# Kernel optimization log

Measured on AMD Instinct MI355X. Metric: run time of the kernel, lower is better.

The kernel has to match this reference:

```python
import jax, jax.numpy as jnp
import numpy as np

DIM = 64
LSH_NUM_PROJS = 7
BLOCK_SIZE = 256
SAMPLE_SIZE = 256
MIN_SEQ_LEN = 2048


def _unit_hamming(n):
    # Gray-code-like permutation used by AngularLSH so adjacent hash ids differ by 1 bit
    a = np.arange(2)
    for i in range(1, n):
        a = np.concatenate([a, a[::-1] + 2 ** i])
    return jnp.asarray(a, dtype=jnp.int32)

_PERM = _unit_hamming(LSH_NUM_PROJS)                                  # [2^P]
_ENC = (2 ** jnp.arange(LSH_NUM_PROJS)).reshape(1, 1, 1, LSH_NUM_PROJS)


def _lsh_hash(mat, proj_dir):
    # mat: [b,h,n,d], proj_dir: [1,1,d,P] -> hash ids [b,h,n]
    mask = jnp.matmul(mat, proj_dir) > 0
    bin_ids = (mask * _ENC).sum(-1)
    return _PERM[bin_ids]


def _exact_attention(q, k, v, scale, causal=False, bias=None):
    qk = jnp.einsum('bhnd,bhmd->bhnm', q, k) * scale
    if causal:
        n, m = q.shape[2], k.shape[2]
        qk = qk + jnp.triu(jnp.full((n, m), jnp.finfo(q.dtype).min, q.dtype), 1)[None, None]
    if bias is not None:
        qk = qk + bias
    lse = jax.scipy.special.logsumexp(qk, axis=-1, keepdims=True)      # [b,h,n,1]
    out = jnp.einsum('bhnm,bhmd->bhnd', jnp.exp(qk - lse), v)
    return out, lse


def _add_attn(a1, l1, a2, l2):
    c = (1.0 / (1.0 + jnp.exp(l2 - l1))).astype(a1.dtype)
    attn = c * a1 + (1 - c) * a2
    lse = l1 - jnp.log(c + jnp.finfo(l1.dtype).eps)
    return attn, lse


def _indexing(x, idx, chunk_size=-1):
    # x: [b,h,n,d], idx: [b,h,s] -> [b,h,s,d] (padded up to a multiple of chunk_size)
    g = jnp.take_along_axis(x, idx[..., None], axis=2)
    n = g.shape[2]
    if chunk_size > 0 and n % chunk_size != 0:
        pad = -n % chunk_size
        g = jnp.pad(g, ((0, 0), (0, 0), (0, pad), (0, 0)))
    return g


def _no_causal(q, k, v, scale, proj_dir, level):
    b, h, n_q, d = q.shape
    n_k = k.shape[2]
    if MIN_SEQ_LEN > n_q:
        return _exact_attention(q, k, v, scale, causal=False)
    q_idx = jnp.argsort(_lsh_hash(q, proj_dir), axis=2)
    k_idx = jnp.argsort(_lsh_hash(k, proj_dir), axis=2)
    q_idx_inv = jnp.argsort(q_idx, axis=2)
    kbs = BLOCK_SIZE
    q_s = _indexing(q, q_idx, kbs)
    k_s = _indexing(k, k_idx, kbs)
    v_s = _indexing(v, k_idx, kbs)
    num_blocks = k_s.shape[2] // kbs
    qbs = q_s.shape[2] // num_blocks
    # block-diagonal attention over LSH-sorted buckets
    q_blk = q_s.reshape(-1, 1, qbs, d)
    k_blk = k_s.reshape(-1, 1, kbs, d)
    v_blk = v_s.reshape(-1, 1, kbs, d)
    attn_block, lse_block = _exact_attention(q_blk, k_blk, v_blk, scale, causal=False)
    attn_block = attn_block.reshape(b, h, q_s.shape[2], -1)
    lse_block = lse_block.reshape(b, h, q_s.shape[2], -1)
    if q_s.shape[2] != n_q:
        attn_block = attn_block[:, :, :n_q, :]
        lse_block = lse_block[:, :, :n_q, :]
        q_s = q_s[:, :, :n_q, :]
        k_s = k_s[:, :, :n_k, :]
        v_s = v_s[:, :, :n_k, :]
    S = SAMPLE_SIZE
    if S > 0 and n_q > qbs and n_k > kbs:
        rng = jax.random.fold_in(jax.random.key(42), level)
        sampled = jax.random.randint(rng, (b, h, S), 0, n_k)
        v_sub = _indexing(v_s, sampled)
        k_sub = _indexing(k_s, sampled)
        offset = jnp.arange(n_q)[None, :, None]                         # (1,n,1)
        bm = (offset // qbs) == (sampled // kbs).reshape(-1, 1, S)      # (b*h,n,S)
        bias = bm.reshape(b, h, n_q, S).astype(q_s.dtype) * jnp.finfo(q_s.dtype).min
        attn_res, lse_res = _exact_attention(q_s, k_sub, v_sub, scale, causal=False, bias=bias)
        lse_res = lse_res + jnp.asarray(np.log(n_k / S), lse_res.dtype)
        attn, lse = _add_attn(attn_block, lse_block, attn_res, lse_res)
    else:
        attn, lse = attn_block, lse_block
    attn = _indexing(attn, q_idx_inv)
    lse = _indexing(lse, q_idx_inv)
    return attn, lse


def _hyper(q, k, v, scale, proj_dir, level=0):
    b, h, n_k, d = k.shape
    n_q = q.shape[2]
    if n_k <= MIN_SEQ_LEN:
        return _exact_attention(q, k, v, scale, causal=True)
    # recursive causal split: block-diagonal halves + un-masked lower-left quadrant
    q_bd = q.reshape(b, 2 * h, n_q // 2, d)
    k_bd = k.reshape(b, 2 * h, n_k // 2, d)
    v_bd = v.reshape(b, 2 * h, n_k // 2, d)
    attn_bd, lse_bd = _hyper(q_bd, k_bd, v_bd, scale, proj_dir, level + 1)
    attn_bd = attn_bd.reshape(b, h, -1, d)
    lse_bd = lse_bd.reshape(b, h, -1, 1)
    a_un, l_un = _no_causal(q[:, :, n_k // 2:, :], k[:, :, :n_k // 2, :],
                            v[:, :, :n_k // 2, :], scale, proj_dir, 100 + level)
    a_up, l_up = attn_bd[:, :, :n_q // 2, :], lse_bd[:, :, :n_q // 2, :]
    a_dn, l_dn = _add_attn(attn_bd[:, :, n_q // 2:, :], lse_bd[:, :, n_q // 2:, :], a_un, l_un)
    return jnp.concatenate([a_up, a_dn], axis=2), jnp.concatenate([l_up, l_dn], axis=2)


def setup_inputs() -> dict:
    rng = jax.random.key(0)
    kq, kk, kv, kp = jax.random.split(rng, 4)
    B, H, N, D = 1, 8, 8192, 64
    return {
        'query': jax.random.normal(kq, (B, H, N, D), jnp.float32),
        'key': jax.random.normal(kk, (B, H, N, D), jnp.float32),
        'value': jax.random.normal(kv, (B, H, N, D), jnp.float32),
        'proj_dir': jax.random.normal(kp, (1, 1, D, LSH_NUM_PROJS), jnp.float32),
    }


def reference(query, key, value, proj_dir):
    scale = query.shape[-1] ** -0.5
    attn, lse = _hyper(query, key, value, scale, proj_dir)
    return attn
```

## Files before the change

kernel.cpp:

```cpp
#include <hip/hip_runtime.h>
#include <stdint.h>
#include <math.h>

#define H 8
#define NSEQ 8192
#define D 64
#define SC2 0.18033688011112042f
#define LN2F 0.69314718055994531f
#define THR2 10.0f
#define EPSF 1.1920928955078125e-07f

typedef short v8s __attribute__((ext_vector_type(8)));
typedef float v4f __attribute__((ext_vector_type(4)));
typedef unsigned short ushort_t;

#define MFMA16(a,b,c) __builtin_amdgcn_mfma_f32_16x16x32_bf16((a),(b),(c),0,0,0)
#define SWZ(row, cb)    (((row)*128) + ((cb) ^ ((((row)&7))<<4)))
#define SWZ256(row, cb) (((row)*256) + ((cb) ^ ((((row)&7))<<4)))

__device__ __forceinline__ float exp2x(float x){
  float r; asm("v_exp_f32 %0, %1" : "=v"(r) : "v"(x)); return r;
}
__device__ __forceinline__ unsigned int cvtpk(float a, float b){
  unsigned int r; asm("v_cvt_pk_bf16_f32 %0, %1, %2" : "=v"(r) : "v"(a), "v"(b)); return r;
}
__device__ __forceinline__ ushort_t f2bf(float f){
  union { float f; unsigned int u; } c; c.f = f;
  unsigned int u = c.u + 0x7FFFu + ((c.u >> 16) & 1u);
  return (ushort_t)(u >> 16);
}
#define VONES (v8s){0x3F80,0x3F80,0x3F80,0x3F80,0x3F80,0x3F80,0x3F80,0x3F80}

__global__ __launch_bounds__(256) void prep_hash(
    const float* __restrict__ q, const float* __restrict__ k, const float* __restrict__ v,
    const float* __restrict__ proj,
    ushort_t* __restrict__ qb, ushort_t* __restrict__ kb, ushort_t* __restrict__ vb,
    int* __restrict__ hq, int* __restrict__ hk)
{
  __shared__ float tile[64][65];
  __shared__ float pj[448];
  __shared__ int pbuf[4][64];
  const int bid = blockIdx.x;
  const int t = threadIdx.x;
  if (bid >= 2048){
    const int tix = bid - 2048;
    size_t off = (size_t)tix*4096 + t*16;
    float4 f0 = *(const float4*)(v + off);
    float4 f1 = *(const float4*)(v + off + 4);
    float4 f2 = *(const float4*)(v + off + 8);
    float4 f3 = *(const float4*)(v + off + 12);
    uint4 o0, o1;
    o0.x = cvtpk(f0.x, f0.y);  o0.y = cvtpk(f0.z, f0.w);
    o0.z = cvtpk(f1.x, f1.y);  o0.w = cvtpk(f1.z, f1.w);
    o1.x = cvtpk(f2.x, f2.y);  o1.y = cvtpk(f2.z, f2.w);
    o1.z = cvtpk(f3.x, f3.y);  o1.w = cvtpk(f3.z, f3.w);
    *(uint4*)(vb + off) = o0;
    *(uint4*)(vb + off + 8) = o1;
    return;
  }
  const int isk = bid & 1;
  const int tix = bid >> 1;
  const int rowbase = tix << 6;
  const float* src = isk ? k : q;
  ushort_t* dstb = isk ? kb : qb;
  int* dsth = isk ? hk : hq;
  for (int i = t; i < 448; i += 256) pj[i] = proj[i];
  {
    const int r = t >> 2, cg = (t & 3) << 4;
    const float* s = src + (size_t)(rowbase + r)*64 + cg;
    float4 f0 = *(const float4*)(s);
    float4 f1 = *(const float4*)(s + 4);
    float4 f2 = *(const float4*)(s + 8);
    float4 f3 = *(const float4*)(s + 12);
    tile[r][cg+0]=f0.x;  tile[r][cg+1]=f0.y;  tile[r][cg+2]=f0.z;  tile[r][cg+3]=f0.w;
    tile[r][cg+4]=f1.x;  tile[r][cg+5]=f1.y;  tile[r][cg+6]=f1.z;  tile[r][cg+7]=f1.w;
    tile[r][cg+8]=f2.x;  tile[r][cg+9]=f2.y;  tile[r][cg+10]=f2.z; tile[r][cg+11]=f2.w;
    tile[r][cg+12]=f3.x; tile[r][cg+13]=f3.y; tile[r][cg+14]=f3.z; tile[r][cg+15]=f3.w;
    uint4 o0, o1;
    o0.x = cvtpk(f0.x, f0.y);  o0.y = cvtpk(f0.z, f0.w);
    o0.z = cvtpk(f1.x, f1.y);  o0.w = cvtpk(f1.z, f1.w);
    o1.x = cvtpk(f2.x, f2.y);  o1.y = cvtpk(f2.z, f2.w);
    o1.z = cvtpk(f3.x, f3.y);  o1.w = cvtpk(f3.z, f3.w);
    *(uint4*)(dstb + (size_t)(rowbase + r)*64 + cg) = o0;
    *(uint4*)(dstb + (size_t)(rowbase + r)*64 + cg + 8) = o1;
  }
  __syncthreads();
  {
    const int r = t & 63, pg = t >> 6;
    const int p2 = (pg < 3) ? (pg + 4) : 6;
    float d0 = 0.0f, d1 = 0.0f;
    for (int d = 0; d < 64; ++d){
      float x = tile[r][d];
      d0 = fmaf(x, pj[d*7 + pg], d0);
      d1 = fmaf(x, pj[d*7 + p2], d1);
    }
    int pb = (d0 > 0.0f ? (1 << pg) : 0);
    if (pg < 3 && d1 > 0.0f) pb |= (1 << (pg + 4));
    pbuf[pg][r] = pb;
  }
  __syncthreads();
  if (t < 64){
    int b = pbuf[0][t] | pbuf[1][t] | pbuf[2][t] | pbuf[3][t];
    dsth[rowbase + t] = b ^ (b >> 1);
  }
}

__device__ __forceinline__ void tf2x32(uint32_t k0, uint32_t k1,
                                       uint32_t x0, uint32_t x1,
                                       uint32_t& o0, uint32_t& o1)
{
  uint32_t ks0 = k0, ks1 = k1, ks2 = k0 ^ k1 ^ 0x1BD11BDAu;
  x0 += ks0; x1 += ks1;
#define RND(r) { x0 += x1; x1 = (x1 << (r)) | (x1 >> (32-(r))); x1 ^= x0; }
  RND(13) RND(15) RND(26) RND(6)  x0 += ks1; x1 += ks2 + 1u;
  RND(17) RND(29) RND(16) RND(24) x0 += ks2; x1 += ks0 + 2u;
  RND(13) RND(15) RND(26) RND(6)  x0 += ks0; x1 += ks1 + 3u;
  RND(17) RND(29) RND(16) RND(24) x0 += ks1; x1 += ks2 + 4u;
  RND(13) RND(15) RND(26) RND(6)  x0 += ks2; x1 += ks0 + 5u;
#undef RND
  o0 = x0; o1 = x1;
}

__device__ __forceinline__ void qk8(const v8s qf[2], const char* Ks, int lo, int hi, v4f sa[8]){
  __builtin_amdgcn_s_setprio(1);
#pragma unroll
  for (int st = 0; st < 8; ++st){
#pragma unroll
    for (int kc = 0; kc < 2; ++kc){
      v8s bf = *(const v8s*)(Ks + SWZ(st*16 + lo, kc*64 + hi*16));
      sa[st] = MFMA16(qf[kc], bf, sa[st]);
    }
  }
  __builtin_amdgcn_s_setprio(0);
}

__device__ __forceinline__ void sm_pv8s(v4f sa[8], char* Pw, const char* VTs,
                                        int lo, int hi, float m[4], v4f o[5]){
  float tm[4];
  bool grow = false;
#pragma unroll
  for (int reg = 0; reg < 4; ++reg){
    float a = fmaxf(fmaxf(sa[0][reg], sa[1][reg]), fmaxf(sa[2][reg], sa[3][reg]));
    float b = fmaxf(fmaxf(sa[4][reg], sa[5][reg]), fmaxf(sa[6][reg], sa[7][reg]));
    tm[reg] = fmaxf(a, b);
    grow = grow || (tm[reg] > m[reg] + THR2);
  }
  if (__any(grow)){
#pragma unroll
    for (int reg = 0; reg < 4; ++reg){
      float t = tm[reg];
      t = fmaxf(t, __shfl_xor(t, 1));
      t = fmaxf(t, __shfl_xor(t, 2));
      t = fmaxf(t, __shfl_xor(t, 4));
      t = fmaxf(t, __shfl_xor(t, 8));
      float mn = fmaxf(m[reg], t);
      float corr = exp2x(m[reg] - mn);
      m[reg] = mn;
#pragma unroll
      for (int dt = 0; dt < 5; ++dt) o[dt][reg] *= corr;
    }
  }
#pragma unroll
  for (int hh = 0; hh < 2; ++hh){
#pragma unroll
    for (int reg = 0; reg < 4; ++reg){
      float mr = m[reg];
      uint2 pw;
      pw.x = cvtpk(exp2x(sa[hh*4+0][reg]-mr), exp2x(sa[hh*4+1][reg]-mr));
      pw.y = cvtpk(exp2x(sa[hh*4+2][reg]-mr), exp2x(sa[hh*4+3][reg]-mr));
      *(uint2*)(Pw + SWZ(hi*4 + reg, 8*lo)) = pw;
    }
    asm volatile("" ::: "memory");
    __builtin_amdgcn_s_setprio(1);
#pragma unroll
    for (int kb = 0; kb < 2; ++kb){
      v8s pa = *(const v8s*)(Pw + SWZ(lo, kb*64 + hi*16));
#pragma unroll
      for (int dt = 0; dt < 4; ++dt){
        v8s vbr = *(const v8s*)(VTs + SWZ256(dt*16 + lo, hh*128 + kb*64 + hi*16));
        o[dt] = MFMA16(pa, vbr, o[dt]);
      }
      o[4] = MFMA16(pa, VONES, o[4]);
    }
    __builtin_amdgcn_s_setprio(0);
    asm volatile("" ::: "memory");
  }
}

__device__ __forceinline__ void vt_write_h(char* VTs, uint2 vr0, uint2 vr1, uint2 vr2, uint2 vr3,
                                           int vdg, int vlo, int vsth){
  const int cb = vsth*128 + vlo*8;
  uint2 w;
  w.x = (vr0.x & 0xFFFFu) | ((vr1.x & 0xFFFFu) << 16);
  w.y = (vr2.x & 0xFFFFu) | ((vr3.x & 0xFFFFu) << 16);
  *(uint2*)(VTs + SWZ256(vdg*4 + 0, cb)) = w;
  w.x = (vr0.x >> 16) | (vr1.x & 0xFFFF0000u);
  w.y = (vr2.x >> 16) | (vr3.x & 0xFFFF0000u);
  *(uint2*)(VTs + SWZ256(vdg*4 + 1, cb)) = w;
  w.x = (vr0.y & 0xFFFFu) | ((vr1.y & 0xFFFFu) << 16);
  w.y = (vr2.y & 0xFFFFu) | ((vr3.y & 0xFFFFu) << 16);
  *(uint2*)(VTs + SWZ256(vdg*4 + 2, cb)) = w;
  w.x = (vr0.y >> 16) | (vr1.y & 0xFFFF0000u);
  w.y = (vr2.y >> 16) | (vr3.y & 0xFFFF0000u);
  *(uint2*)(VTs + SWZ256(vdg*4 + 3, cb)) = w;
}

__global__ __launch_bounds__(512, 4) void diag_sort(
    const ushort_t* __restrict__ qb, const ushort_t* __restrict__ kb, const ushort_t* __restrict__ vb,
    float* __restrict__ out, float* __restrict__ lse,
    const int* __restrict__ hq, const int* __restrict__ hk,
    int* __restrict__ q100, int* __restrict__ k100,
    int* __restrict__ q101, int* __restrict__ k101,
    int* __restrict__ s100, int* __restrict__ s101)
{
  __shared__ __align__(16) char lds[49664];
  const int bid0 = blockIdx.x;
  const int tid = threadIdx.x;

  if (bid0 >= 512){
    const int sbid = bid0 - 512;
    unsigned char  (*hist)[128] = (unsigned char (*)[128])lds;
    unsigned short (*off )[128] = (unsigned short(*)[128])(lds + 16384);
    int* bstart = (int*)(lds + 49152);
    const int t = tid;
    if (t < 128){
      int gid = sbid*128 + t;
      int level, span, idx; int* outp;
      if (gid < 2048){ level = 100; span = 4096; outp = s100; idx = gid; }
      else           { level = 101; span = 2048; outp = s101; idx = gid - 2048; }
      uint32_t r0, r1; tf2x32(0u, 42u, 0u, (uint32_t)level, r0, r1);
      uint32_t k20, k21; tf2x32(r0, r1, 0u, 1u, k20, k21);
      uint32_t o0, o1; tf2x32(k20, k21, 0u, (uint32_t)idx, o0, o1);
      outp[idx] = (int)((o0 ^ o1) % (uint32_t)span);
    }
    const int* src = nullptr; int n = 0, base = 0; int* outp = nullptr;
    if (sbid < 8)       { int h = sbid;     src = hq + h*NSEQ + 4096;        n = 4096; base = 4096;          outp = q100 + h*4096; }
    else if (sbid < 16) { int h = sbid - 8; src = hk + h*NSEQ;               n = 4096; base = 0;             outp = k100 + h*4096; }
    else if (sbid < 32) { int id = sbid-16; int h = id>>1, p = id&1;
                          src = hq + h*NSEQ + p*4096 + 2048;                 n = 2048; base = p*4096 + 2048; outp = q101 + id*2048; }
    else                { int id = sbid-32; int h = id>>1, p = id&1;
                          src = hk + h*NSEQ + p*4096;                        n = 2048; base = p*4096;       outp = k101 + id*2048; }
    const int chunk = n >> 7;
    if (t < 128) for (int b = 0; b < 128; ++b) hist[t][b] = 0;
    __syncthreads();
    const int* mysrc = src + (t & 127) * chunk;
    if (t < 128) for (int i = 0; i < chunk; ++i) hist[t][mysrc[i]]++;
    __syncthreads();
    if (t < 128){
      int s = 0;
      for (int tt = 0; tt < 128; ++tt) s += hist[tt][t];
      bstart[t] = s;
    }
    __syncthreads();
    if (t == 0){
      int run = 0;
      for (int b = 0; b < 128; ++b){ int c = bstart[b]; bstart[b] = run; run += c; }
    }
    __syncthreads();
    if (t < 128){
      unsigned int run = (unsigned int)bstart[t];
      for (int tt = 0; tt < 128; ++tt){ off[tt][t] = (unsigned short)run; run += hist[tt][t]; }
    }
    __syncthreads();
    if (t < 128){
      for (int i = 0; i < chunk; ++i){
        int hsh = mysrc[i];
        unsigned short pos = off[t][hsh]++;
        outp[pos] = base + t * chunk + i;
      }
    }
    return;
  }

  char* Ks  = lds;
  char* VTs = lds + 16384;
  char* Ps  = lds + 32768;
  int j;
  if (bid0 < 256) j = 15 - (bid0 >> 5);
  else            j = (bid0 - 256) >> 5;
  const int inst = bid0 & 31;
  const int h = inst >> 2, tblk = inst & 3;
  const size_t hoff = (size_t)h * NSEQ * D;
  const ushort_t* qh = qb + hoff; const ushort_t* kh = kb + hoff; const ushort_t* vh = vb + hoff;
  const int blkbase = tblk * 2048;
  const int w = tid >> 6, lane = tid & 63;
  const int lo = lane & 15, hi = lane >> 4;
  char* Pw = Ps + w*2048;
  const int kr = tid >> 2, kq = tid & 3;
  const int vlo = tid & 15, vdg = (tid >> 4) & 15, vsth = tid >> 8;

  const int qt = (w < 4) ? (2*j + 1) : (2*j);
  const int nkt = j + 1;
  const int qpos0 = qt*64 + (w & 3)*16;

  v8s qf[2];
  {
    const ushort_t* r = qh + (size_t)(blkbase + qpos0 + lo) * D;
    qf[0] = *(const v8s*)(r + hi*8);
    qf[1] = *(const v8s*)(r + 32 + hi*8);
  }
  const v4f vz = {0.0f, 0.0f, 0.0f, 0.0f};
  v4f o[5] = {vz, vz, vz, vz, vz};
  float m[4] = {-INFINITY, -INFINITY, -INFINITY, -INFINITY};

  uint4 kreg0, kreg1; uint2 vr0, vr1, vr2, vr3;
#define DLOAD(kt) { \
    const ushort_t* ksr = kh + (size_t)(blkbase + (kt)*128 + kr)*D + kq*16; \
    kreg0 = *(const uint4*)ksr; \
    kreg1 = *(const uint4*)(ksr + 8); \
    const ushort_t* vs = vh + (size_t)(blkbase + (kt)*128 + vsth*64 + vlo)*D + vdg*4; \
    vr0 = *(const uint2*)(vs); \
    vr1 = *(const uint2*)(vs + 16*D); \
    vr2 = *(const uint2*)(vs + 32*D); \
    vr3 = *(const uint2*)(vs + 48*D); }

  DLOAD(0);
#pragma unroll 1
  for (int kt = 0; kt < nkt; ++kt){
    *(uint4*)(Ks + SWZ(kr, kq*32))      = kreg0;
    *(uint4*)(Ks + SWZ(kr, kq*32 + 16)) = kreg1;
    vt_write_h(VTs, vr0, vr1, vr2, vr3, vdg, vlo, vsth);
    __syncthreads();
    if (kt + 1 < nkt) DLOAD(kt+1);
    {
      v4f sa[8] = {vz, vz, vz, vz, vz, vz, vz, vz};
      qk8(qf, Ks, lo, hi, sa);
#pragma unroll
      for (int st = 0; st < 8; ++st) sa[st] *= SC2;
      if (kt == nkt - 1){
#pragma unroll
        for (int st = 0; st < 8; ++st){
          int kpos = kt*128 + st*16 + lo;
#pragma unroll
          for (int reg = 0; reg < 4; ++reg)
            if (kpos > qpos0 + hi*4 + reg) sa[st][reg] = -INFINITY;
        }
      }
      sm_pv8s(sa, Pw, VTs, lo, hi, m, o);
    }
    __syncthreads();
  }
#undef DLOAD
#pragma unroll
  for (int reg = 0; reg < 4; ++reg){
    int rw = blkbase + qpos0 + hi*4 + reg;
    float lsum = o[4][reg];
    float inv = 1.0f / lsum;
#pragma unroll
    for (int dt = 0; dt < 4; ++dt)
      out[hoff + (size_t)rw*D + dt*16 + lo] = o[dt][reg] * inv;
    if (lo == 0) lse[h*NSEQ + rw] = m[reg]*LN2F + logf(lsum);
  }
}

__global__ __launch_bounds__(512, 4) void nc_both(
    const ushort_t* __restrict__ qb, const ushort_t* __restrict__ kb, const ushort_t* __restrict__ vb,
    float* __restrict__ out, float* __restrict__ lse,
    const int* __restrict__ q101, const int* __restrict__ k101, const int* __restrict__ s101,
    const int* __restrict__ q100, const int* __restrict__ k100, const int* __restrict__ s100,
    ushort_t* __restrict__ a100, float* __restrict__ lse100)
{
  __shared__ __align__(16) char Ks[16384];
  __shared__ __align__(16) char VTs[16384];
  __shared__ __align__(16) char Ps[8][2048];
  __shared__ unsigned int ilds[512];
  const int bid = blockIdx.x;
  const bool lvl101 = bid < 256;
  int inst, jb; float delta2; int seglen;
  const int *qi, *ki, *sp;
  if (lvl101){
    int xcd = bid & 7, sl = bid >> 3; inst = xcd*2 + (sl >> 4); jb = sl & 15;
    delta2 = 3.0f; seglen = 2048;
    qi = q101 + inst*seglen; ki = k101 + inst*seglen; sp = s101 + inst*256;
  } else {
    int b2 = bid - 256; inst = b2 & 7; jb = b2 >> 3;
    delta2 = 4.0f; seglen = 4096;
    qi = q100 + inst*seglen; ki = k100 + inst*seglen; sp = s100 + inst*256;
  }
  const int h = lvl101 ? (inst >> 1) : inst;
  const int qblk = jb >> 1;
  const size_t hoff = (size_t)h * NSEQ * D;
  const ushort_t* qh = qb + hoff; const ushort_t* kh = kb + hoff; const ushort_t* vh = vb + hoff;
  const int tid = threadIdx.x;
  const int w = tid >> 6, lane = tid & 63;
  const int lo = lane & 15, hi = lane >> 4;
  char* Pw = Ps[w];
  const int kr = tid >> 2, kq = tid & 3;
  const int vlo = tid & 15, vdg = (tid >> 4) & 15, vsth = tid >> 8;

  {
    if (tid < 256){
      ilds[tid] = (unsigned int)ki[qblk*256 + tid];
    } else {
      int s = sp[tid - 256];
      unsigned int krow = (unsigned int)ki[s];
      if ((s >> 8) == qblk) krow |= 0x80000000u;
      ilds[tid] = krow;
    }
  }
  int orig[4];
  v8s qf[2];
  {
    int qrl = qi[jb*128 + w*16 + lo];
    const ushort_t* r = qh + (size_t)qrl * D;
    qf[0] = *(const v8s*)(r + hi*8);
    qf[1] = *(const v8s*)(r + 32 + hi*8);
#pragma unroll
    for (int reg = 0; reg < 4; ++reg) orig[reg] = qi[jb*128 + w*16 + hi*4 + reg];
  }
  const v4f vz = {0.0f, 0.0f, 0.0f, 0.0f};
  v4f o[5] = {vz, vz, vz, vz, vz};
  float m[4] = {-INFINITY, -INFINITY, -INFINITY, -INFINITY};
  __syncthreads();

  uint4 kreg0, kreg1; uint2 vr0, vr1, vr2, vr3;
#define NLOAD(kt) { \
    unsigned int krow = ilds[(kt)*128 + kr] & 0x7FFFFFFFu; \
    const ushort_t* ksr = kh + (size_t)krow*D + kq*16; \
    kreg0 = *(const uint4*)ksr; \
    kreg1 = *(const uint4*)(ksr + 8); \
    unsigned int g0 = ilds[(kt)*128 + vsth*64 + vlo     ] & 0x7FFFFFFFu; \
    unsigned int g1 = ilds[(kt)*128 + vsth*64 + 16 + vlo] & 0x7FFFFFFFu; \
    unsigned int g2 = ilds[(kt)*128 + vsth*64 + 32 + vlo] & 0x7FFFFFFFu; \
    unsigned int g3 = ilds[(kt)*128 + vsth*64 + 48 + vlo] & 0x7FFFFFFFu; \
    vr0 = *(const uint2*)(vh + (size_t)g0*D + vdg*4); \
    vr1 = *(const uint2*)(vh + (size_t)g1*D + vdg*4); \
    vr2 = *(const uint2*)(vh + (size_t)g2*D + vdg*4); \
    vr3 = *(const uint2*)(vh + (size_t)g3*D + vdg*4); }

  NLOAD(0);
#pragma unroll 1
  for (int kt = 0; kt < 4; ++kt){
    *(uint4*)(Ks + SWZ(kr, kq*32))      = kreg0;
    *(uint4*)(Ks + SWZ(kr, kq*32 + 16)) = kreg1;
    vt_write_h(VTs, vr0, vr1, vr2, vr3, vdg, vlo, vsth);
    __syncthreads();
    if (kt + 1 < 4) NLOAD(kt+1);
    v4f sa[8] = {vz, vz, vz, vz, vz, vz, vz, vz};
    qk8(qf, Ks, lo, hi, sa);
    if (kt < 2){
#pragma unroll
      for (int st = 0; st < 8; ++st) sa[st] *= SC2;
    } else {
#pragma unroll
      for (int st = 0; st < 8; ++st){
        if (ilds[kt*128 + st*16 + lo] >> 31) sa[st] = (v4f){-INFINITY, -INFINITY, -INFINITY, -INFINITY};
        else                                 sa[st] = sa[st]*SC2 + delta2;
      }
    }
    sm_pv8s(sa, Pw, VTs, lo, hi, m, o);
    __syncthreads();
  }
#undef NLOAD
  if (lvl101){
#pragma unroll
    for (int reg = 0; reg < 4; ++reg){
      int og = orig[reg];
      float lsum = o[4][reg];
      float l1v = lse[h*NSEQ + og];
      float l2v = m[reg]*LN2F + logf(lsum);
      float c = 1.0f / (1.0f + __expf(l2v - l1v));
      float inv = (1.0f - c) / lsum;
#pragma unroll
      for (int dt = 0; dt < 4; ++dt){
        float* ap = out + hoff + (size_t)og*D + dt*16 + lo;
        *ap = c * (*ap) + inv * o[dt][reg];
      }
      if (lo == 0) lse[h*NSEQ + og] = l1v - logf(c + EPSF);
    }
  } else {
#pragma unroll
    for (int reg = 0; reg < 4; ++reg){
      int og = orig[reg];
      float lsum = o[4][reg];
      float inv = 1.0f / lsum;
      ushort_t* arow = a100 + ((size_t)h*NSEQ + og)*D;
#pragma unroll
      for (int dt = 0; dt < 4; ++dt)
        arow[dt*16 + lo] = f2bf(o[dt][reg] * inv);
      if (lo == 0) lse100[h*NSEQ + og] = m[reg]*LN2F + logf(lsum);
    }
  }
}

__global__ __launch_bounds__(256) void merge_kernel(
    float* __restrict__ out, const float* __restrict__ lse,
    const ushort_t* __restrict__ a100, const float* __restrict__ lse100)
{
  const int gid = blockIdx.x * 256 + threadIdx.x;
  const size_t e = (size_t)gid * 4;
  const int h = (int)(e >> 18);
  const int rem = (int)(e & 262143);
  const int og = 4096 + (rem >> 6);
  const size_t row = (size_t)h*NSEQ + og;
  const float l1 = lse[row];
  const float l2 = lse100[row];
  const float c = 1.0f / (1.0f + __expf(l2 - l1));
  const float ic = 1.0f - c;
  float* op = out + ((size_t)h*NSEQ*D) + (size_t)og*D + (rem & 63);
  float4 ov = *(float4*)op;
  uint2 av = *(const uint2*)(a100 + row*D + (rem & 63));
  float a0 = __uint_as_float((av.x & 0xFFFFu) << 16);
  float a1 = __uint_as_float((av.x & 0xFFFF0000u));
  float a2 = __uint_as_float((av.y & 0xFFFFu) << 16);
  float a3 = __uint_as_float((av.y & 0xFFFF0000u));
  ov.x = c*ov.x + ic*a0;
  ov.y = c*ov.y + ic*a1;
  ov.z = c*ov.z + ic*a2;
  ov.w = c*ov.w + ic*a3;
  *(float4*)op = ov;
}

extern "C" void kernel_launch(void* const* d_in, const int* in_sizes, int n_in,
                              void* d_out, int out_size, void* d_ws, size_t ws_size,
                              hipStream_t stream)
{
  const float* q    = (const float*)d_in[0];
  const float* k    = (const float*)d_in[1];
  const float* v    = (const float*)d_in[2];
  const float* proj = (const float*)d_in[3];
  float* out = (float*)d_out;

  char* ws = (char*)d_ws;
  float* lse = (float*)ws;
  int* hq   = (int*)(ws + 262144);
  int* hk   = (int*)(ws + 524288);
  int* q100 = (int*)(ws + 786432);
  int* k100 = (int*)(ws + 917504);
  int* q101 = (int*)(ws + 1048576);
  int* k101 = (int*)(ws + 1179648);
  int* s100 = (int*)(ws + 1310720);
  int* s101 = (int*)(ws + 1318912);
  ushort_t* qb = (ushort_t*)(ws + 1335296);
  ushort_t* kb = qb + (size_t)H*NSEQ*D;
  ushort_t* vb = kb + (size_t)H*NSEQ*D;
  ushort_t* a100 = vb + (size_t)H*NSEQ*D;
  float* lse100 = (float*)(a100 + (size_t)H*NSEQ*D);

  prep_hash    <<<dim3(3072), dim3(256), 0, stream>>>(q, k, v, proj, qb, kb, vb, hq, hk);
  diag_sort    <<<dim3(560),  dim3(512), 0, stream>>>(qb, kb, vb, out, lse, hq, hk,
                                                      q100, k100, q101, k101, s100, s101);
  nc_both      <<<dim3(512),  dim3(512), 0, stream>>>(qb, kb, vb, out, lse,
                                                      q101, k101, s101, q100, k100, s100,
                                                      a100, lse100);
  merge_kernel <<<dim3(2048), dim3(256), 0, stream>>>(out, lse, a100, lse100);
}
```

Baseline: 100.0 us.

## Split long causal diagonal tiles across two blocks and merge partial results

Causal diagonal tiles with j>=8 are now split into two key-range chunks handled by separate blocks. One chunk writes to the a100/lse100 scratch and a new dmerge kernel combines the halves with a log-sum-exp merge, which is meant to balance the uneven per-block work of the triangle. To avoid clobbering that scratch, nc_both now merges level-100 rows below 6144 directly into out, and only the remaining rows go to scratch for a smaller merge_kernel. The cost is an extra kernel launch, more scratch traffic, and bf16 rounding of the partial results.

```diff
diff --git a/kernel.cpp b/kernel.cpp
--- a/kernel.cpp
+++ b/kernel.cpp
@@ -211,14 +211,15 @@
     const int* __restrict__ hq, const int* __restrict__ hk,
     int* __restrict__ q100, int* __restrict__ k100,
     int* __restrict__ q101, int* __restrict__ k101,
-    int* __restrict__ s100, int* __restrict__ s101)
+    int* __restrict__ s100, int* __restrict__ s101,
+    ushort_t* __restrict__ a100, float* __restrict__ lse100)
 {
   __shared__ __align__(16) char lds[49664];
   const int bid0 = blockIdx.x;
   const int tid = threadIdx.x;
 
-  if (bid0 >= 512){
-    const int sbid = bid0 - 512;
+  if (bid0 >= 768){
+    const int sbid = bid0 - 768;
     unsigned char  (*hist)[128] = (unsigned char (*)[128])lds;
     unsigned short (*off )[128] = (unsigned short(*)[128])(lds + 16384);
     int* bstart = (int*)(lds + 49152);
@@ -275,10 +276,22 @@
   char* Ks  = lds;
   char* VTs = lds + 16384;
   char* Ps  = lds + 32768;
-  int j;
-  if (bid0 < 256) j = 15 - (bid0 >> 5);
-  else            j = (bid0 - 256) >> 5;
-  const int inst = bid0 & 31;
+  int inst, j, kt0, kt1;
+  bool toscratch;
+  if (bid0 < 512){
+    const int idx = bid0;
+    j = 15 - (idx >> 6);
+    const int chunkA = (idx >> 5) & 1;
+    inst = idx & 31;
+    const int h1 = (j + 1) >> 1;
+    if (chunkA){ kt0 = 0;  kt1 = h1;     toscratch = true;  }
+    else       { kt0 = h1; kt1 = j + 1;  toscratch = false; }
+  } else {
+    const int idx = bid0 - 512;
+    j = 7 - (idx >> 5);
+    inst = idx & 31;
+    kt0 = 0; kt1 = j + 1; toscratch = false;
+  }
   const int h = inst >> 2, tblk = inst & 3;
   const size_t hoff = (size_t)h * NSEQ * D;
   const ushort_t* qh = qb + hoff; const ushort_t* kh = kb + hoff; const ushort_t* vh = vb + hoff;
@@ -290,7 +303,6 @@
   const int vlo = tid & 15, vdg = (tid >> 4) & 15, vsth = tid >> 8;
 
   const int qt = (w < 4) ? (2*j + 1) : (2*j);
-  const int nkt = j + 1;
   const int qpos0 = qt*64 + (w & 3)*16;
 
   v8s qf[2];
@@ -314,20 +326,20 @@
     vr2 = *(const uint2*)(vs + 32*D); \
     vr3 = *(const uint2*)(vs + 48*D); }
 
-  DLOAD(0);
+  DLOAD(kt0);
 #pragma unroll 1
-  for (int kt = 0; kt < nkt; ++kt){
+  for (int kt = kt0; kt < kt1; ++kt){
     *(uint4*)(Ks + SWZ(kr, kq*32))      = kreg0;
     *(uint4*)(Ks + SWZ(kr, kq*32 + 16)) = kreg1;
     vt_write_h(VTs, vr0, vr1, vr2, vr3, vdg, vlo, vsth);
     __syncthreads();
-    if (kt + 1 < nkt) DLOAD(kt+1);
+    if (kt + 1 < kt1) DLOAD(kt+1);
     {
       v4f sa[8] = {vz, vz, vz, vz, vz, vz, vz, vz};
       qk8(qf, Ks, lo, hi, sa);
 #pragma unroll
       for (int st = 0; st < 8; ++st) sa[st] *= SC2;
-      if (kt == nkt - 1){
+      if (kt == j){
 #pragma unroll
         for (int st = 0; st < 8; ++st){
           int kpos = kt*128 + st*16 + lo;
@@ -341,16 +353,64 @@
     __syncthreads();
   }
 #undef DLOAD
-#pragma unroll
-  for (int reg = 0; reg < 4; ++reg){
-    int rw = blkbase + qpos0 + hi*4 + reg;
-    float lsum = o[4][reg];
-    float inv = 1.0f / lsum;
-#pragma unroll
-    for (int dt = 0; dt < 4; ++dt)
-      out[hoff + (size_t)rw*D + dt*16 + lo] = o[dt][reg] * inv;
-    if (lo == 0) lse[h*NSEQ + rw] = m[reg]*LN2F + logf(lsum);
-  }
+  if (!toscratch){
+#pragma unroll
+    for (int reg = 0; reg < 4; ++reg){
+      int rw = blkbase + qpos0 + hi*4 + reg;
+      float lsum = o[4][reg];
+      float inv = 1.0f / lsum;
+#pragma unroll
+      for (int dt = 0; dt < 4; ++dt)
+        out[hoff + (size_t)rw*D + dt*16 + lo] = o[dt][reg] * inv;
+      if (lo == 0) lse[h*NSEQ + rw] = m[reg]*LN2F + logf(lsum);
+    }
+  } else {
+#pragma unroll
+    for (int reg = 0; reg < 4; ++reg){
+      int rw = blkbase + qpos0 + hi*4 + reg;
+      float lsum = o[4][reg];
+      float inv = 1.0f / lsum;
+      ushort_t* arow = a100 + ((size_t)h*NSEQ + rw)*D;
+#pragma unroll
+      for (int dt = 0; dt < 4; ++dt)
+        arow[dt*16 + lo] = f2bf(o[dt][reg] * inv);
+      if (lo == 0) lse100[h*NSEQ + rw] = m[reg]*LN2F + logf(lsum);
+    }
+  }
+}
+
+__global__ __launch_bounds__(256) void dmerge(
+    float* __restrict__ out, float* __restrict__ lse,
+    const ushort_t* __restrict__ a100, const float* __restrict__ lse100)
+{
+  const int gid = blockIdx.x * 256 + threadIdx.x;
+  const size_t e = (size_t)gid * 4;
+  const int h = (int)(e >> 18);
+  const int rem = (int)(e & 262143);
+  const int tblk = rem >> 16;
+  const int r2 = (rem >> 6) & 1023;
+  const int dd = rem & 63;
+  const int row = tblk*2048 + 1024 + r2;
+  const size_t grow = (size_t)h*NSEQ + row;
+  const float l1 = lse[grow];
+  const float l2 = lse100[grow];
+  const float mx = fmaxf(l1, l2);
+  const float w1 = __expf(l1 - mx), w2 = __expf(l2 - mx);
+  const float inv = 1.0f / (w1 + w2);
+  const float c1 = w1 * inv, c2 = w2 * inv;
+  float* op = out + (size_t)h*NSEQ*D + (size_t)row*D + dd;
+  float4 ov = *(float4*)op;
+  uint2 av = *(const uint2*)(a100 + grow*D + dd);
+  float a0 = __uint_as_float((av.x & 0xFFFFu) << 16);
+  float a1 = __uint_as_float((av.x & 0xFFFF0000u));
+  float a2 = __uint_as_float((av.y & 0xFFFFu) << 16);
+  float a3 = __uint_as_float((av.y & 0xFFFF0000u));
+  ov.x = c1*ov.x + c2*a0;
+  ov.y = c1*ov.y + c2*a1;
+  ov.z = c1*ov.z + c2*a2;
+  ov.w = c1*ov.w + c2*a3;
+  *(float4*)op = ov;
+  if (dd == 0) lse[grow] = mx + logf(w1 + w2);
 }
 
 __global__ __launch_bounds__(512, 4) void nc_both(
@@ -452,11 +512,11 @@
     __syncthreads();
   }
 #undef NLOAD
-  if (lvl101){
-#pragma unroll
-    for (int reg = 0; reg < 4; ++reg){
-      int og = orig[reg];
-      float lsum = o[4][reg];
+#pragma unroll
+  for (int reg = 0; reg < 4; ++reg){
+    int og = orig[reg];
+    float lsum = o[4][reg];
+    if (lvl101 || og < 6144){
       float l1v = lse[h*NSEQ + og];
       float l2v = m[reg]*LN2F + logf(lsum);
       float c = 1.0f / (1.0f + __expf(l2v - l1v));
@@ -467,12 +527,7 @@
         *ap = c * (*ap) + inv * o[dt][reg];
       }
       if (lo == 0) lse[h*NSEQ + og] = l1v - logf(c + EPSF);
-    }
-  } else {
-#pragma unroll
-    for (int reg = 0; reg < 4; ++reg){
-      int og = orig[reg];
-      float lsum = o[4][reg];
+    } else {
       float inv = 1.0f / lsum;
       ushort_t* arow = a100 + ((size_t)h*NSEQ + og)*D;
 #pragma unroll
@@ -489,9 +544,9 @@
 {
   const int gid = blockIdx.x * 256 + threadIdx.x;
   const size_t e = (size_t)gid * 4;
-  const int h = (int)(e >> 18);
-  const int rem = (int)(e & 262143);
-  const int og = 4096 + (rem >> 6);
+  const int h = (int)(e >> 17);
+  const int rem = (int)(e & 131071);
+  const int og = 6144 + (rem >> 6);
   const size_t row = (size_t)h*NSEQ + og;
   const float l1 = lse[row];
   const float l2 = lse100[row];
@@ -538,10 +593,12 @@
   float* lse100 = (float*)(a100 + (size_t)H*NSEQ*D);
 
   prep_hash    <<<dim3(3072), dim3(256), 0, stream>>>(q, k, v, proj, qb, kb, vb, hq, hk);
-  diag_sort    <<<dim3(560),  dim3(512), 0, stream>>>(qb, kb, vb, out, lse, hq, hk,
-                                                      q100, k100, q101, k101, s100, s101);
+  diag_sort    <<<dim3(816),  dim3(512), 0, stream>>>(qb, kb, vb, out, lse, hq, hk,
+                                                      q100, k100, q101, k101, s100, s101,
+                                                      a100, lse100);
+  dmerge       <<<dim3(2048), dim3(256), 0, stream>>>(out, lse, a100, lse100);
   nc_both      <<<dim3(512),  dim3(512), 0, stream>>>(qb, kb, vb, out, lse,
                                                       q101, k101, s101, q100, k100, s100,
                                                       a100, lse100);
-  merge_kernel <<<dim3(2048), dim3(256), 0, stream>>>(out, lse, a100, lse100);
-}
+  merge_kernel <<<dim3(1024), dim3(256), 0, stream>>>(out, lse, a100, lse100);
+}
```

After: 110.2 us. 10.2% more time.
